# Kernel optimization log

Hardware: AMD Instinct MI355X
Metric: run time of the kernel (lower is better)

The kernel has to match this reference:

```python
import jax, jax.numpy as jnp
import numpy as np

B, T, D, H = 2, 2048, 1024, 16
HS = D // H
EPS = 1e-5


def setup_inputs() -> dict:
    key = jax.random.key(0)
    ks = jax.random.split(key, 16)
    s = lambda *shape: 0.02
    inp = {
        "x": jax.random.normal(ks[0], (B, T, D), jnp.float32),
        # per-head Q/K/V weights stacked over heads: [H, D, HS]
        "Wq": jax.random.normal(ks[1], (H, D, HS), jnp.float32) * 0.02,
        "bq": jnp.zeros((H, HS), jnp.float32),
        "Wk": jax.random.normal(ks[2], (H, D, HS), jnp.float32) * 0.02,
        "bk": jnp.zeros((H, HS), jnp.float32),
        "Wv": jax.random.normal(ks[3], (H, D, HS), jnp.float32) * 0.02,
        "bv": jnp.zeros((H, HS), jnp.float32),
        "Wp": jax.random.normal(ks[4], (D, D), jnp.float32) * 0.02,
        "bp": jnp.zeros((D,), jnp.float32),
        "W1": jax.random.normal(ks[5], (D, 4 * D), jnp.float32) * 0.02,
        "b1": jnp.zeros((4 * D,), jnp.float32),
        "W2": jax.random.normal(ks[6], (4 * D, D), jnp.float32) * 0.02,
        "b2": jnp.zeros((D,), jnp.float32),
        "g1": jnp.ones((D,), jnp.float32),
        "be1": jnp.zeros((D,), jnp.float32),
        "g2": jnp.ones((D,), jnp.float32),
        "be2": jnp.zeros((D,), jnp.float32),
    }
    return inp


def layernorm(x, g, b):
    mu = jnp.mean(x, axis=-1, keepdims=True)
    var = jnp.mean(jnp.square(x - mu), axis=-1, keepdims=True)
    return (x - mu) * jax.lax.rsqrt(var + EPS) * g + b


def reference(x, Wq, bq, Wk, bk, Wv, bv, Wp, bp, W1, b1, W2, b2, g1, be1, g2, be2):
    # NOTE: this block applies LN then residual-adds the *normalized* x,
    # exactly as in the original (x = ln1(x); x = x + mha(x)).
    h = layernorm(x, g1, be1)
    # multi-head attention, all heads batched via stacked weights
    q = jnp.einsum('btd,hdk->bhtk', h, Wq) + bq[None, :, None, :]
    k = jnp.einsum('btd,hdk->bhtk', h, Wk) + bk[None, :, None, :]
    v = jnp.einsum('btd,hdk->bhtk', h, Wv) + bv[None, :, None, :]
    att = jnp.einsum('bhtk,bhsk->bhts', q, k) * (HS ** -0.5)  # [B,H,T,T]
    att = jax.nn.softmax(att, axis=-1)
    o = jnp.einsum('bhts,bhsk->bhtk', att, v)  # [B,H,T,HS]
    # concat heads in order along last dim -> [B,T,D]
    o = jnp.transpose(o, (0, 2, 1, 3)).reshape(B, T, D)
    o = o @ Wp + bp
    h = h + o
    h2 = layernorm(h, g2, be2)
    ff = jax.nn.gelu(h2 @ W1 + b1, approximate=False) @ W2 + b2
    return h2 + ff
```

## Files before the change

### kernel.cpp

```cpp
#include <hip/hip_runtime.h>
#include <cstdint>
#include <cstddef>

#define B_  2
#define T_  2048
#define D_  1024
#define H_  16
#define HS_ 64
#define MTOT (B_*T_)

typedef unsigned short u16;
typedef __attribute__((ext_vector_type(8))) __bf16 bf16x8;
typedef __attribute__((ext_vector_type(4))) float f32x4;

__device__ __forceinline__ u16 f2bf(float f) {
  unsigned int u = __builtin_bit_cast(unsigned int, f);
  u += 0x7fffu + ((u >> 16) & 1u);
  return (u16)(u >> 16);
}

__device__ __forceinline__ unsigned cvtpk(float lo, float hi) {
  unsigned r;
  asm("v_cvt_pk_bf16_f32 %0, %1, %2" : "=v"(r) : "v"(lo), "v"(hi));
  return r;
}

__device__ __forceinline__ void gload16(const u16* g, u16* l) {
  __builtin_amdgcn_global_load_lds((const __attribute__((address_space(1))) void*)g,
                                   (__attribute__((address_space(3))) void*)l, 16, 0, 0);
}

__global__ __launch_bounds__(256) void transpose_f2b(const float* __restrict__ in,
                                                     u16* __restrict__ out, int R, int C) {
  __shared__ float tile[32][33];
  int c0 = blockIdx.x * 32, r0 = blockIdx.y * 32;
  size_t zoff = (size_t)blockIdx.z * R * C;
  const float* src = in + zoff;
  u16* dst = out + zoff;
  int tx = threadIdx.x & 31, ty = threadIdx.x >> 5;
#pragma unroll
  for (int k = 0; k < 4; ++k)
    tile[ty + k*8][tx] = src[(size_t)(r0 + ty + k*8) * C + c0 + tx];
  __syncthreads();
#pragma unroll
  for (int k = 0; k < 4; ++k)
    dst[(size_t)(c0 + ty + k*8) * R + r0 + tx] = f2bf(tile[tx][ty + k*8]);
}

__global__ __launch_bounds__(256) void transpose_v(const u16* __restrict__ in,
                                                   u16* __restrict__ out) {
  __shared__ u16 tile[32][33];
  int z = blockIdx.z;
  int b = z >> 4, h = z & 15;
  int t0 = blockIdx.x * 32, f0 = blockIdx.y * 32;
  int tx = threadIdx.x & 31, ty = threadIdx.x >> 5;
#pragma unroll
  for (int k = 0; k < 4; ++k)
    tile[ty + k*8][tx] = in[((size_t)b*T_ + t0 + ty + k*8) * D_ + h*HS_ + f0 + tx];
  __syncthreads();
#pragma unroll
  for (int k = 0; k < 4; ++k)
    out[((size_t)z*HS_ + f0 + ty + k*8) * T_ + t0 + tx] = tile[tx][ty + k*8];
}

__global__ __launch_bounds__(256) void ln_kernel(const float* __restrict__ x,
                                                 const float* __restrict__ gg,
                                                 const float* __restrict__ be,
                                                 float* __restrict__ hf,
                                                 u16* __restrict__ hb) {
  int row = blockIdx.x;
  int t = threadIdx.x;
  const float* xr = x + (size_t)row * D_;
  float4 xv = *(const float4*)&xr[t * 4];
  float s  = xv.x + xv.y + xv.z + xv.w;
  float ss = xv.x*xv.x + xv.y*xv.y + xv.z*xv.z + xv.w*xv.w;
#pragma unroll
  for (int m = 1; m < 64; m <<= 1) { s += __shfl_xor(s, m); ss += __shfl_xor(ss, m); }
  __shared__ float red[8];
  int lane = t & 63, wv = t >> 6;
  if (lane == 0) { red[wv] = s; red[4 + wv] = ss; }
  __syncthreads();
  s  = red[0] + red[1] + red[2] + red[3];
  ss = red[4] + red[5] + red[6] + red[7];
  float mu  = s * (1.0f / D_);
  float var = ss * (1.0f / D_) - mu * mu;
  float rs  = rsqrtf(var + 1e-5f);
  float4 gv = *(const float4*)&gg[t * 4];
  float4 bv = *(const float4*)&be[t * 4];
  float4 hv;
  hv.x = (xv.x - mu) * rs * gv.x + bv.x;
  hv.y = (xv.y - mu) * rs * gv.y + bv.y;
  hv.z = (xv.z - mu) * rs * gv.z + bv.z;
  hv.w = (xv.w - mu) * rs * gv.w + bv.w;
  *(float4*)&hf[(size_t)row * D_ + t * 4] = hv;
  uint2 pk;
  pk.x = (unsigned)f2bf(hv.x) | ((unsigned)f2bf(hv.y) << 16);
  pk.y = (unsigned)f2bf(hv.z) | ((unsigned)f2bf(hv.w) << 16);
  *(uint2*)&hb[(size_t)row * D_ + t * 4] = pk;
}

template<int EPI>
__global__ __launch_bounds__(256) void gemm_bt(
    const u16* __restrict__ A, const u16* __restrict__ Bt,
    const float* __restrict__ bias0, const float* __restrict__ bias1,
    const float* __restrict__ bias2, const float* __restrict__ res,
    float* __restrict__ outf, u16* __restrict__ o0, u16* __restrict__ o1,
    u16* __restrict__ o2, int M, int N, int K) {
  __shared__ __align__(16) u16 As[2][128 * 32];
  __shared__ __align__(16) u16 Bs[2][128 * 32];
  const int tid = threadIdx.x;
  const int lane = tid & 63, wv = tid >> 6;
  const int m0 = blockIdx.y * 128, n0 = blockIdx.x * 128;
  const int rA = lane & 15, g = lane >> 4;
  const int wm = (wv >> 1) * 64, wn = (wv & 1) * 64;
  const int sx = (rA >> 1) & 3;

  f32x4 acc[4][4] = {};

  auto stage = [&](int tt, int bufi) {
#pragma unroll
    for (int p = 0; p < 2; ++p) {
      int c = (p * 4 + wv) * 64 + lane;
      int row = c >> 2;
      int s = (c & 3) ^ ((row >> 1) & 3);
      gload16(A  + (size_t)(m0 + row) * K + tt * 32 + s * 8,
              &As[bufi][0] + (size_t)(p * 4 + wv) * 512);
      gload16(Bt + (size_t)(n0 + row) * K + tt * 32 + s * 8,
              &Bs[bufi][0] + (size_t)(p * 4 + wv) * 512);
    }
  };

  stage(0, 0);

  const int nk = K >> 5;
  for (int t = 0; t < nk; ++t) {
    __syncthreads();
    const int buf = t & 1;
    if (t + 1 < nk) stage(t + 1, buf ^ 1);

    bf16x8 a[4], b[4];
#pragma unroll
    for (int i = 0; i < 4; ++i)
      a[i] = *(const bf16x8*)&As[buf][(wm + i * 16 + rA) * 32 + ((g ^ sx) << 3)];
#pragma unroll
    for (int i = 0; i < 4; ++i)
      b[i] = *(const bf16x8*)&Bs[buf][(wn + i * 16 + rA) * 32 + ((g ^ sx) << 3)];
#pragma unroll
    for (int i = 0; i < 4; ++i)
#pragma unroll
      for (int j = 0; j < 4; ++j)
        acc[i][j] = __builtin_amdgcn_mfma_f32_16x16x32_bf16(a[i], b[j], acc[i][j], 0, 0, 0);
  }

#pragma unroll
  for (int i = 0; i < 4; ++i) {
#pragma unroll
    for (int j = 0; j < 4; ++j) {
#pragma unroll
      for (int r = 0; r < 4; ++r) {
        int row = m0 + wm + i * 16 + g * 4 + r;
        int col = n0 + wn + j * 16 + rA;
        float v = acc[i][j][r];
        if constexpr (EPI == 0) {
          int sel = col >> 10, nn = col & 1023;
          const float* bp = sel == 0 ? bias0 : (sel == 1 ? bias1 : bias2);
          u16* op = sel == 0 ? o0 : (sel == 1 ? o1 : o2);
          op[(size_t)row * 1024 + nn] = f2bf(v + bp[nn]);
        } else if constexpr (EPI == 1) {
          v += bias0[col];
          v = 0.5f * v * (1.0f + erff(v * 0.70710678118f));
          o0[(size_t)row * N + col] = f2bf(v);
        } else {
          v += bias0[col] + res[(size_t)row * N + col];
          outf[(size_t)row * N + col] = v;
        }
      }
    }
  }
}

__global__ __launch_bounds__(256) void attn_kernel(const u16* __restrict__ qg,
                                                   const u16* __restrict__ kg,
                                                   const u16* __restrict__ vtg,
                                                   u16* __restrict__ og) {
  const int wg = blockIdx.x;
  const int qt = wg & 31;
  const int h  = (wg >> 5) & 15;
  const int b  = wg >> 9;
  const int tid = threadIdx.x, lane = tid & 63, wv = tid >> 6;
  const int q0 = qt * 64 + wv * 16;
  const int rA = lane & 15, g = lane >> 4;
  const int rx = rA & 7;

  __shared__ __align__(16) u16 Ks[2][64 * 64];
  __shared__ __align__(16) u16 Vs[2][64 * 64];
  __shared__ __align__(16) u16 Ps[4][16 * 64];

  const size_t qoff = ((size_t)b * T_ + q0 + rA) * D_ + h * HS_ + g * 8;
  const bf16x8 aq0 = *(const bf16x8*)&qg[qoff];
  const bf16x8 aq1 = *(const bf16x8*)&qg[qoff + 32];

  const u16* kbase = kg + (size_t)b * T_ * D_ + h * HS_;
  const u16* vbase = vtg + ((size_t)b * H_ + h) * HS_ * T_;

  const float cfold = 0.18033688011112042f;
  float mrun = -1e30f, lrun = 0.0f;
  f32x4 oacc[4] = {};

  auto stage = [&](int t, int buf) {
#pragma unroll
    for (int p = 0; p < 2; ++p) {
      int chunk = p * 256 + wv * 64 + lane;
      int row = chunk >> 3, s = chunk & 7;
      int ss = s ^ (row & 7);
      gload16(kbase + ((size_t)t * 64 + row) * D_ + ss * 8,
              &Ks[buf][0] + (size_t)(p * 256 + wv * 64) * 8);
      gload16(vbase + (size_t)row * T_ + t * 64 + ss * 8,
              &Vs[buf][0] + (size_t)(p * 256 + wv * 64) * 8);
    }
  };

  stage(0, 0);

  const int NT = T_ / 64;
  for (int t = 0; t < NT; ++t) {
    __syncthreads();
    const int buf = t & 1;
    if (t + 1 < NT) stage(t + 1, buf ^ 1);

    const u16* kb = &Ks[buf][0];
    f32x4 sc[4];
    __builtin_amdgcn_s_setprio(1);
#pragma unroll
    for (int st = 0; st < 4; ++st) {
      bf16x8 k0 = *(const bf16x8*)&kb[(st * 16 + rA) * 64 + ((g ^ rx) << 3)];
      bf16x8 k1 = *(const bf16x8*)&kb[(st * 16 + rA) * 64 + (((4 + g) ^ rx) << 3)];
      f32x4 z = {};
      z = __builtin_amdgcn_mfma_f32_16x16x32_bf16(k0, aq0, z, 0, 0, 0);
      z = __builtin_amdgcn_mfma_f32_16x16x32_bf16(k1, aq1, z, 0, 0, 0);
      sc[st] = z;
    }
    __builtin_amdgcn_s_setprio(0);

    float a0 = fmaxf(fmaxf(sc[0][0], sc[0][1]), fmaxf(sc[0][2], sc[0][3]));
    float a1 = fmaxf(fmaxf(sc[1][0], sc[1][1]), fmaxf(sc[1][2], sc[1][3]));
    float a2 = fmaxf(fmaxf(sc[2][0], sc[2][1]), fmaxf(sc[2][2], sc[2][3]));
    float a3 = fmaxf(fmaxf(sc[3][0], sc[3][1]), fmaxf(sc[3][2], sc[3][3]));
    float mx = fmaxf(fmaxf(a0, a1), fmaxf(a2, a3));
    mx = fmaxf(mx, __shfl_xor(mx, 16));
    mx = fmaxf(mx, __shfl_xor(mx, 32));
    float tm = mx * cfold;

    if (__any(tm > mrun + 8.0f)) {
      float mnew = fmaxf(mrun, tm);
      float sca = __builtin_amdgcn_exp2f(mrun - mnew);
      mrun = mnew;
      lrun *= sca;
#pragma unroll
      for (int f = 0; f < 4; ++f) oacc[f] *= sca;
    }

    float p[16];
#pragma unroll
    for (int st = 0; st < 4; ++st)
#pragma unroll
      for (int r = 0; r < 4; ++r)
        p[st * 4 + r] = __builtin_amdgcn_exp2f(__builtin_fmaf(sc[st][r], cfold, -mrun));

    float sum = (((p[0] + p[1]) + (p[2] + p[3])) + ((p[4] + p[5]) + (p[6] + p[7])))
              + (((p[8] + p[9]) + (p[10] + p[11])) + ((p[12] + p[13]) + (p[14] + p[15])));
    sum += __shfl_xor(sum, 16);
    sum += __shfl_xor(sum, 32);
    lrun += sum;

    char* psb = (char*)&Ps[wv][0];
#pragma unroll
    for (int st = 0; st < 4; ++st) {
      uint2 w;
      w.x = cvtpk(p[st * 4 + 0], p[st * 4 + 1]);
      w.y = cvtpk(p[st * 4 + 2], p[st * 4 + 3]);
      int slot = st * 2 + (g >> 1);
      *(uint2*)&psb[rA * 128 + (((slot ^ rx)) << 4) + ((g & 1) << 3)] = w;
    }
    bf16x8 pf0 = *(const bf16x8*)&psb[rA * 128 + ((g ^ rx) << 4)];
    bf16x8 pf1 = *(const bf16x8*)&psb[rA * 128 + (((4 + g) ^ rx) << 4)];

    const u16* vbl = &Vs[buf][0];
    __builtin_amdgcn_s_setprio(1);
#pragma unroll
    for (int f = 0; f < 4; ++f) {
      bf16x8 v0 = *(const bf16x8*)&vbl[(f * 16 + rA) * 64 + ((g ^ rx) << 3)];
      bf16x8 v1 = *(const bf16x8*)&vbl[(f * 16 + rA) * 64 + (((4 + g) ^ rx) << 3)];
      oacc[f] = __builtin_amdgcn_mfma_f32_16x16x32_bf16(v0, pf0, oacc[f], 0, 0, 0);
      oacc[f] = __builtin_amdgcn_mfma_f32_16x16x32_bf16(v1, pf1, oacc[f], 0, 0, 0);
    }
    __builtin_amdgcn_s_setprio(0);
  }

  float linv = 1.0f / lrun;
#pragma unroll
  for (int f = 0; f < 4; ++f) {
    uint2 w;
    w.x = cvtpk(oacc[f][0] * linv, oacc[f][1] * linv);
    w.y = cvtpk(oacc[f][2] * linv, oacc[f][3] * linv);
    *(uint2*)&og[((size_t)b * T_ + q0 + rA) * D_ + h * HS_ + f * 16 + g * 4] = w;
  }
}

extern "C" void kernel_launch(void* const* d_in, const int* in_sizes, int n_in,
                              void* d_out, int out_size, void* d_ws, size_t ws_size,
                              hipStream_t stream) {
  const float* x   = (const float*)d_in[0];
  const float* Wq  = (const float*)d_in[1];
  const float* bq  = (const float*)d_in[2];
  const float* Wk  = (const float*)d_in[3];
  const float* bk  = (const float*)d_in[4];
  const float* Wv  = (const float*)d_in[5];
  const float* bv  = (const float*)d_in[6];
  const float* Wp  = (const float*)d_in[7];
  const float* bp  = (const float*)d_in[8];
  const float* W1  = (const float*)d_in[9];
  const float* b1  = (const float*)d_in[10];
  const float* W2  = (const float*)d_in[11];
  const float* b2  = (const float*)d_in[12];
  const float* g1  = (const float*)d_in[13];
  const float* be1 = (const float*)d_in[14];
  const float* g2  = (const float*)d_in[15];
  const float* be2 = (const float*)d_in[16];
  float* out = (float*)d_out;

  char* w = (char*)d_ws;
  auto alloc = [&](size_t bytes) { char* p = w; w += (bytes + 255) & ~(size_t)255; return p; };
  const size_t MD = (size_t)MTOT * D_;

  float* h_f    = (float*)alloc(MD * 4);
  u16*   h_b    = (u16*)  alloc(MD * 2);
  u16*   wqkv_t = (u16*)  alloc(3 * (size_t)D_ * D_ * 2);
  u16*   wp_t   = (u16*)  alloc((size_t)D_ * D_ * 2);
  u16*   w1_t   = (u16*)  alloc((size_t)D_ * 4 * D_ * 2);
  u16*   w2_t   = (u16*)  alloc((size_t)D_ * 4 * D_ * 2);
  u16*   q_b    = (u16*)  alloc(MD * 2);
  u16*   k_b    = (u16*)  alloc(MD * 2);
  u16*   v_b    = (u16*)  alloc(MD * 2);
  u16*   vt_b   = (u16*)  alloc(MD * 2);
  u16*   o_b    = (u16*)  alloc(MD * 2);
  float* hat_f  = (float*)alloc(MD * 4);
  u16*   ff1_b  = q_b;
  float* h2_f   = h_f;
  u16*   h2_b   = h_b;

  dim3 blk(256);

  transpose_f2b<<<dim3(2, 32, 16), blk, 0, stream>>>(Wq, wqkv_t, 1024, 64);
  transpose_f2b<<<dim3(2, 32, 16), blk, 0, stream>>>(Wk, wqkv_t + (size_t)D_ * D_, 1024, 64);
  transpose_f2b<<<dim3(2, 32, 16), blk, 0, stream>>>(Wv, wqkv_t + 2 * (size_t)D_ * D_, 1024, 64);
  transpose_f2b<<<dim3(32, 32, 1), blk, 0, stream>>>(Wp, wp_t, 1024, 1024);
  transpose_f2b<<<dim3(128, 32, 1), blk, 0, stream>>>(W1, w1_t, 1024, 4096);
  transpose_f2b<<<dim3(32, 128, 1), blk, 0, stream>>>(W2, w2_t, 4096, 1024);

  ln_kernel<<<dim3(MTOT), blk, 0, stream>>>(x, g1, be1, h_f, h_b);

  gemm_bt<0><<<dim3(24, 32), blk, 0, stream>>>(h_b, wqkv_t, bq, bk, bv,
      nullptr, nullptr, q_b, k_b, v_b, MTOT, 3072, 1024);

  transpose_v<<<dim3(64, 2, 32), blk, 0, stream>>>(v_b, vt_b);

  attn_kernel<<<dim3(B_ * H_ * (T_ / 64)), blk, 0, stream>>>(q_b, k_b, vt_b, o_b);

  gemm_bt<2><<<dim3(8, 32), blk, 0, stream>>>(o_b, wp_t, bp, nullptr, nullptr,
      h_f, hat_f, nullptr, nullptr, nullptr, MTOT, 1024, 1024);

  ln_kernel<<<dim3(MTOT), blk, 0, stream>>>(hat_f, g2, be2, h2_f, h2_b);

  gemm_bt<1><<<dim3(32, 32), blk, 0, stream>>>(h2_b, w1_t, b1, nullptr, nullptr,
      nullptr, nullptr, ff1_b, nullptr, nullptr, MTOT, 4096, 1024);

  gemm_bt<2><<<dim3(8, 32), blk, 0, stream>>>(ff1_b, w2_t, b2, nullptr, nullptr,
      h2_f, out, nullptr, nullptr, nullptr, MTOT, 1024, 4096);
}
```

Before: 309.3 us.

## Triple-buffer GEMM loads, split-K the FF2 GEMM, use tanh-form GELU

The GEMM mainloop moves from double to triple buffering. It uses explicit vmcnt waits and a raw barrier so global loads run two stages ahead of the MFMAs. The FF2 GEMM is split along K into two z-slices that write fp32 partials, and a new reduce kernel adds the partials, bias and residual. The first FFN GEMM's exact erf GELU is replaced by a tanh-approximation computed via exp2. The split-K path spends extra memory traffic on partial buffers to gain parallelism, and the GELU approximation changes numerics slightly.

```diff
diff --git a/kernel.cpp b/kernel.cpp
--- a/kernel.cpp
+++ b/kernel.cpp
@@ -105,12 +105,13 @@
     const float* __restrict__ bias0, const float* __restrict__ bias1,
     const float* __restrict__ bias2, const float* __restrict__ res,
     float* __restrict__ outf, u16* __restrict__ o0, u16* __restrict__ o1,
-    u16* __restrict__ o2, int M, int N, int K) {
-  __shared__ __align__(16) u16 As[2][128 * 32];
-  __shared__ __align__(16) u16 Bs[2][128 * 32];
+    u16* __restrict__ o2, int M, int N, int K, int kLen) {
+  __shared__ __align__(16) u16 As[3][128 * 32];
+  __shared__ __align__(16) u16 Bs[3][128 * 32];
   const int tid = threadIdx.x;
   const int lane = tid & 63, wv = tid >> 6;
   const int m0 = blockIdx.y * 128, n0 = blockIdx.x * 128;
+  const int kOff = blockIdx.z * kLen;
   const int rA = lane & 15, g = lane >> 4;
   const int wm = (wv >> 1) * 64, wn = (wv & 1) * 64;
   const int sx = (rA >> 1) & 3;
@@ -123,33 +124,40 @@
       int c = (p * 4 + wv) * 64 + lane;
       int row = c >> 2;
       int s = (c & 3) ^ ((row >> 1) & 3);
-      gload16(A  + (size_t)(m0 + row) * K + tt * 32 + s * 8,
+      gload16(A  + (size_t)(m0 + row) * K + kOff + tt * 32 + s * 8,
               &As[bufi][0] + (size_t)(p * 4 + wv) * 512);
-      gload16(Bt + (size_t)(n0 + row) * K + tt * 32 + s * 8,
+      gload16(Bt + (size_t)(n0 + row) * K + kOff + tt * 32 + s * 8,
               &Bs[bufi][0] + (size_t)(p * 4 + wv) * 512);
     }
   };
 
+  const int nk = kLen >> 5;
   stage(0, 0);
-
-  const int nk = K >> 5;
+  stage(1, 1);
+
+  int cur = 0, nxt = 2;
   for (int t = 0; t < nk; ++t) {
-    __syncthreads();
-    const int buf = t & 1;
-    if (t + 1 < nk) stage(t + 1, buf ^ 1);
+    if (t + 1 < nk) asm volatile("s_waitcnt vmcnt(4)" ::: "memory");
+    else            asm volatile("s_waitcnt vmcnt(0)" ::: "memory");
+    __builtin_amdgcn_s_barrier();
+    __builtin_amdgcn_sched_barrier(0);
+    if (t + 2 < nk) stage(t + 2, nxt);
 
     bf16x8 a[4], b[4];
 #pragma unroll
     for (int i = 0; i < 4; ++i)
-      a[i] = *(const bf16x8*)&As[buf][(wm + i * 16 + rA) * 32 + ((g ^ sx) << 3)];
+      a[i] = *(const bf16x8*)&As[cur][(wm + i * 16 + rA) * 32 + ((g ^ sx) << 3)];
 #pragma unroll
     for (int i = 0; i < 4; ++i)
-      b[i] = *(const bf16x8*)&Bs[buf][(wn + i * 16 + rA) * 32 + ((g ^ sx) << 3)];
+      b[i] = *(const bf16x8*)&Bs[cur][(wn + i * 16 + rA) * 32 + ((g ^ sx) << 3)];
 #pragma unroll
     for (int i = 0; i < 4; ++i)
 #pragma unroll
       for (int j = 0; j < 4; ++j)
         acc[i][j] = __builtin_amdgcn_mfma_f32_16x16x32_bf16(a[i], b[j], acc[i][j], 0, 0, 0);
+
+    cur = (cur == 2) ? 0 : cur + 1;
+    nxt = (nxt == 2) ? 0 : nxt + 1;
   }
 
 #pragma unroll
@@ -168,15 +176,39 @@
           op[(size_t)row * 1024 + nn] = f2bf(v + bp[nn]);
         } else if constexpr (EPI == 1) {
           v += bias0[col];
-          v = 0.5f * v * (1.0f + erff(v * 0.70710678118f));
+          float z = 0.7978845608f * (v + 0.044715f * v * v * v);
+          z = fminf(z, 18.0f);
+          float e = __builtin_amdgcn_exp2f(z * 2.8853900817779268f);
+          v = v * e / (e + 1.0f);
           o0[(size_t)row * N + col] = f2bf(v);
-        } else {
+        } else if constexpr (EPI == 2) {
           v += bias0[col] + res[(size_t)row * N + col];
           outf[(size_t)row * N + col] = v;
+        } else {
+          float* dst = blockIdx.z ? (float*)o1 : outf;
+          dst[(size_t)row * N + col] = v;
         }
       }
     }
   }
+}
+
+__global__ __launch_bounds__(256) void reduce_ff2(const float* __restrict__ p0,
+                                                  const float* __restrict__ p1,
+                                                  const float* __restrict__ bias,
+                                                  const float* __restrict__ res,
+                                                  float* __restrict__ out) {
+  int i = (blockIdx.x * 256 + threadIdx.x) * 4;
+  float4 a = *(const float4*)&p0[i];
+  float4 b = *(const float4*)&p1[i];
+  float4 r = *(const float4*)&res[i];
+  float4 bb = *(const float4*)&bias[i & 1023];
+  float4 o;
+  o.x = a.x + b.x + r.x + bb.x;
+  o.y = a.y + b.y + r.y + bb.y;
+  o.z = a.z + b.z + r.z + bb.z;
+  o.w = a.w + b.w + r.w + bb.w;
+  *(float4*)&out[i] = o;
 }
 
 __global__ __launch_bounds__(256) void attn_kernel(const u16* __restrict__ qg,
@@ -348,6 +380,8 @@
   u16*   ff1_b  = q_b;
   float* h2_f   = h_f;
   u16*   h2_b   = h_b;
+  float* pf0    = hat_f;
+  float* pf1    = (float*)h_b;
 
   dim3 blk(256);
 
@@ -360,21 +394,23 @@
 
   ln_kernel<<<dim3(MTOT), blk, 0, stream>>>(x, g1, be1, h_f, h_b);
 
-  gemm_bt<0><<<dim3(24, 32), blk, 0, stream>>>(h_b, wqkv_t, bq, bk, bv,
-      nullptr, nullptr, q_b, k_b, v_b, MTOT, 3072, 1024);
+  gemm_bt<0><<<dim3(24, 32, 1), blk, 0, stream>>>(h_b, wqkv_t, bq, bk, bv,
+      nullptr, nullptr, q_b, k_b, v_b, MTOT, 3072, 1024, 1024);
 
   transpose_v<<<dim3(64, 2, 32), blk, 0, stream>>>(v_b, vt_b);
 
   attn_kernel<<<dim3(B_ * H_ * (T_ / 64)), blk, 0, stream>>>(q_b, k_b, vt_b, o_b);
 
-  gemm_bt<2><<<dim3(8, 32), blk, 0, stream>>>(o_b, wp_t, bp, nullptr, nullptr,
-      h_f, hat_f, nullptr, nullptr, nullptr, MTOT, 1024, 1024);
+  gemm_bt<2><<<dim3(8, 32, 1), blk, 0, stream>>>(o_b, wp_t, bp, nullptr, nullptr,
+      h_f, hat_f, nullptr, nullptr, nullptr, MTOT, 1024, 1024, 1024);
 
   ln_kernel<<<dim3(MTOT), blk, 0, stream>>>(hat_f, g2, be2, h2_f, h2_b);
 
-  gemm_bt<1><<<dim3(32, 32), blk, 0, stream>>>(h2_b, w1_t, b1, nullptr, nullptr,
-      nullptr, nullptr, ff1_b, nullptr, nullptr, MTOT, 4096, 1024);
-
-  gemm_bt<2><<<dim3(8, 32), blk, 0, stream>>>(ff1_b, w2_t, b2, nullptr, nullptr,
-      h2_f, out, nullptr, nullptr, nullptr, MTOT, 1024, 4096);
-}
+  gemm_bt<1><<<dim3(32, 32, 1), blk, 0, stream>>>(h2_b, w1_t, b1, nullptr, nullptr,
+      nullptr, nullptr, ff1_b, nullptr, nullptr, MTOT, 4096, 1024, 1024);
+
+  gemm_bt<3><<<dim3(8, 32, 2), blk, 0, stream>>>(ff1_b, w2_t, nullptr, nullptr,
+      nullptr, nullptr, pf0, nullptr, (u16*)pf1, nullptr, MTOT, 1024, 4096, 2048);
+
+  reduce_ff2<<<dim3(MTOT), blk, 0, stream>>>(pf0, pf1, b2, h2_f, out);
+}
```

After: 289.7 us. -6.3%, faster.
